# Kernel tuning notes

Measured on AMD Instinct MI355X. Metric: run time of the kernel, lower is better.

## Reference

```python
import jax, jax.numpy as jnp
import numpy as np


def fwht(x):
    """Unnormalized Fast Walsh-Hadamard transform along axis 0 (Sylvester order).
    Equivalent to H @ x where H is the +/-1 Hadamard matrix. x.shape[0] must be a power of 2."""
    D = x.shape[0]
    orig_shape = x.shape
    x = x.reshape(D, -1)
    h = 1
    while h < D:
        x = x.reshape(D // (2 * h), 2, h, -1)
        a = x[:, 0]
        b = x[:, 1]
        x = jnp.stack([a + b, a - b], axis=1)
        h *= 2
    return x.reshape(orig_shape)


def setup_inputs() -> dict:
    D = 4096
    B = 2048
    key = jax.random.key(0)
    k_x, k_eps, k_rho = jax.random.split(key, 3)
    x = jax.random.normal(k_x, (B, D), dtype=jnp.float32)
    epsilon = jax.random.normal(k_eps, (D,), dtype=jnp.float32)
    s1 = jnp.ones((D,), dtype=jnp.float32) * 0.01
    s2 = jnp.ones((D,), dtype=jnp.float32) * 0.01
    g_mu = jnp.zeros((D,), dtype=jnp.float32)
    # g_rho ~ Uniform(-5, -4) as in the torch init
    g_rho = jax.random.uniform(k_rho, (D,), dtype=jnp.float32, minval=-5.0, maxval=-4.0)
    return {"x": x, "epsilon": epsilon, "s1": s1, "s2": s2, "g_mu": g_mu, "g_rho": g_rho}


def reference(x, epsilon, s1, s2, g_mu, g_rho):
    D = s1.shape[0]
    # g_sigma_sqrt_diagonal = softplus(g_rho); sampled diag g = g_mu + sigma * eps.
    # W = diag(s1) @ H @ diag(g) @ H @ diag(s2); mu and sigma terms are linear in g, so combine.
    g = g_mu + jax.nn.softplus(g_rho) * epsilon
    # HS2 = H * s2 (columns of H scaled by s2) = H @ diag(s2) = fwht(diag(s2)) along axis 0
    HS2 = fwht(jnp.diag(s2))                      # [D, D]
    W = s1[:, None] * fwht(g[:, None] * HS2)      # [D, D]
    # F.linear(x, W) = x @ W^T
    return x @ W.T
```

## Files before the change

### kernel.cpp

```cpp
#include <hip/hip_runtime.h>
#include <math.h>

#define DIM 4096
#define ROWS 2048
#define LSTR 65

__device__ __forceinline__ float4 f4mul(float4 a, float4 b) {
    return make_float4(a.x * b.x, a.y * b.y, a.z * b.z, a.w * b.w);
}

__device__ __forceinline__ void fwht_ri(float4 v[16]) {
#pragma unroll
    for (int j = 0; j < 16; ++j) {
        float4 a = v[j];
        float t0 = a.x + a.y, t1 = a.x - a.y;
        float t2 = a.z + a.w, t3 = a.z - a.w;
        v[j] = make_float4(t0 + t2, t1 + t3, t0 - t2, t1 - t3);
    }
#pragma unroll
    for (int m = 1; m < 16; m <<= 1) {
#pragma unroll
        for (int j = 0; j < 16; ++j) {
            if (!(j & m)) {
                int k = j | m;
                float4 a = v[j], b = v[k];
                v[j] = make_float4(a.x + b.x, a.y + b.y, a.z + b.z, a.w + b.w);
                v[k] = make_float4(a.x - b.x, a.y - b.y, a.z - b.z, a.w - b.w);
            }
        }
    }
}

__device__ __forceinline__ void fwht_m(float f[64]) {
#pragma unroll
    for (int s = 0; s < 6; ++s) {
        const int h = 1 << s;
#pragma unroll
        for (int m = 0; m < 64; ++m) {
            if (!(m & h)) {
                const int k = m | h;
                float a = f[m], b = f[k];
                f[m] = a + b;
                f[k] = a - b;
            }
        }
    }
}

__global__ void __launch_bounds__(256, 2)
whvi_main(const float* __restrict__ x, const float* __restrict__ s1,
          const float* __restrict__ s2, const float* __restrict__ eps,
          const float* __restrict__ g_mu, const float* __restrict__ g_rho,
          float* __restrict__ out) {
    const int lane = threadIdx.x & 63;
    const int wid  = threadIdx.x >> 6;
    const int row  = blockIdx.x * 4 + wid;

    __shared__ float lds[4 * 64 * LSTR];
    float* __restrict__ L = lds + wid * 64 * LSTR;

    const float4* __restrict__ xr  = (const float4*)(x + (size_t)row * DIM);
    float4* __restrict__       orw = (float4*)(out + (size_t)row * DIM);
    const float4* __restrict__ s2v = (const float4*)s2;
    const float4* __restrict__ s1v = (const float4*)s1;

    float f[64];
    float4* F = (float4*)f;

#pragma unroll
    for (int r = 0; r < 16; ++r)
        F[r] = f4mul(xr[64 * r + lane], s2v[64 * r + lane]);

    fwht_ri(F);

#pragma unroll
    for (int c = 0; c < 64; ++c)
        L[lane * LSTR + c] = f[c];
#pragma unroll
    for (int m = 0; m < 64; ++m)
        f[m] = L[m * LSTR + lane];

    fwht_m(f);

    {
        const int base = 256 * (lane >> 2) + (lane & 3);
#pragma unroll
        for (int m = 0; m < 64; ++m) {
            const int j = base + 4 * m;
            float u  = __expf(g_rho[j]);
            float sp = __logf(1.0f + u);
            f[m] *= fmaf(sp, eps[j], g_mu[j]);
        }
    }

    fwht_m(f);

#pragma unroll
    for (int m = 0; m < 64; ++m)
        L[lane * LSTR + m] = f[m];
#pragma unroll
    for (int c = 0; c < 64; ++c)
        f[c] = L[c * LSTR + lane];

    fwht_ri(F);

#pragma unroll
    for (int r = 0; r < 16; ++r)
        orw[64 * r + lane] = f4mul(F[r], s1v[64 * r + lane]);
}

extern "C" void kernel_launch(void* const* d_in, const int* in_sizes, int n_in,
                              void* d_out, int out_size, void* d_ws, size_t ws_size,
                              hipStream_t stream) {
    const float* x     = (const float*)d_in[0];
    const float* eps   = (const float*)d_in[1];
    const float* s1    = (const float*)d_in[2];
    const float* s2    = (const float*)d_in[3];
    const float* g_mu  = (const float*)d_in[4];
    const float* g_rho = (const float*)d_in[5];
    float* out = (float*)d_out;

    whvi_main<<<ROWS / 4, 256, 0, stream>>>(x, s1, s2, eps, g_mu, g_rho, out);
}
```

Measured before the change: 106.1 us.

## Precompute diagonal g in a pre-pass kernel and vectorize LDS transposes

A small kernel now computes the diagonal g = g_mu + softplus(g_rho)*eps once, stored in workspace in a lane-contiguous permuted layout. The main kernel reads it as float4 instead of redoing exp/log and three strided scalar loads per element in every row. The LDS row stride changes from 65 to 68 so the row-wise stores can use 128-bit writes, and the occupancy hint in launch_bounds is dropped. The cost is an extra kernel launch, a workspace dependency, and possible bank conflicts on the column reads with the new stride.

```diff
diff --git a/kernel.cpp b/kernel.cpp
--- a/kernel.cpp
+++ b/kernel.cpp
@@ -3,7 +3,18 @@
 
 #define DIM 4096
 #define ROWS 2048
-#define LSTR 65
+#define LSTR 68
+
+__global__ void g_precompute(const float* __restrict__ eps,
+                             const float* __restrict__ g_mu,
+                             const float* __restrict__ g_rho,
+                             float* __restrict__ g_t) {
+    int t = blockIdx.x * blockDim.x + threadIdx.x;
+    int l = t >> 6, m = t & 63;
+    int j = 256 * (l >> 2) + 4 * m + (l & 3);
+    float sp = log1pf(expf(g_rho[j]));
+    g_t[t] = g_mu[j] + sp * eps[j];
+}
 
 __device__ __forceinline__ float4 f4mul(float4 a, float4 b) {
     return make_float4(a.x * b.x, a.y * b.y, a.z * b.z, a.w * b.w);
@@ -47,10 +58,9 @@
     }
 }
 
-__global__ void __launch_bounds__(256, 2)
+__global__ void __launch_bounds__(256)
 whvi_main(const float* __restrict__ x, const float* __restrict__ s1,
-          const float* __restrict__ s2, const float* __restrict__ eps,
-          const float* __restrict__ g_mu, const float* __restrict__ g_rho,
+          const float* __restrict__ s2, const float* __restrict__ g_t,
           float* __restrict__ out) {
     const int lane = threadIdx.x & 63;
     const int wid  = threadIdx.x >> 6;
@@ -58,11 +68,13 @@
 
     __shared__ float lds[4 * 64 * LSTR];
     float* __restrict__ L = lds + wid * 64 * LSTR;
+    float4* __restrict__ L4 = (float4*)(L);
 
     const float4* __restrict__ xr  = (const float4*)(x + (size_t)row * DIM);
     float4* __restrict__       orw = (float4*)(out + (size_t)row * DIM);
     const float4* __restrict__ s2v = (const float4*)s2;
     const float4* __restrict__ s1v = (const float4*)s1;
+    const float4* __restrict__ gtv = (const float4*)g_t;
 
     float f[64];
     float4* F = (float4*)f;
@@ -74,30 +86,23 @@
     fwht_ri(F);
 
 #pragma unroll
-    for (int c = 0; c < 64; ++c)
-        L[lane * LSTR + c] = f[c];
+    for (int r = 0; r < 16; ++r)
+        L4[lane * (LSTR / 4) + r] = F[r];
 #pragma unroll
     for (int m = 0; m < 64; ++m)
         f[m] = L[m * LSTR + lane];
 
     fwht_m(f);
 
-    {
-        const int base = 256 * (lane >> 2) + (lane & 3);
 #pragma unroll
-        for (int m = 0; m < 64; ++m) {
-            const int j = base + 4 * m;
-            float u  = __expf(g_rho[j]);
-            float sp = __logf(1.0f + u);
-            f[m] *= fmaf(sp, eps[j], g_mu[j]);
-        }
-    }
+    for (int k = 0; k < 16; ++k)
+        F[k] = f4mul(F[k], gtv[lane * 16 + k]);
 
     fwht_m(f);
 
 #pragma unroll
-    for (int m = 0; m < 64; ++m)
-        L[lane * LSTR + m] = f[m];
+    for (int k = 0; k < 16; ++k)
+        L4[lane * (LSTR / 4) + k] = F[k];
 #pragma unroll
     for (int c = 0; c < 64; ++c)
         f[c] = L[c * LSTR + lane];
@@ -119,6 +124,8 @@
     const float* g_mu  = (const float*)d_in[4];
     const float* g_rho = (const float*)d_in[5];
     float* out = (float*)d_out;
+    float* g_t = (float*)d_ws;
 
-    whvi_main<<<ROWS / 4, 256, 0, stream>>>(x, s1, s2, eps, g_mu, g_rho, out);
+    g_precompute<<<DIM / 256, 256, 0, stream>>>(eps, g_mu, g_rho, g_t);
+    whvi_main<<<ROWS / 4, 256, 0, stream>>>(x, s1, s2, g_t, out);
 }
```

Result: no change. 104.3 us (-1.7%).

## Precompute diagonal g into shared memory, vectorize LDS writes, shrink blocks

Applied to the files above, without the earlier changes.

Each block now computes the sampled diagonal g (softplus of g_rho times eps plus g_mu) once into a padded shared-memory table. The per-element strided global loads and transcendentals in the scaling step become LDS reads. The transpose stride is padded to 68 so register rows can be written as float4. Blocks drop to two waves of 128 threads with no min-blocks hint, and the g table is recomputed per block, which adds redundant exp/log work and a barrier.

```diff
diff --git a/kernel.cpp b/kernel.cpp
--- a/kernel.cpp
+++ b/kernel.cpp
@@ -3,7 +3,10 @@
 
 #define DIM 4096
 #define ROWS 2048
-#define LSTR 65
+#define LSTR 68
+
+#define GPAD(e) ((e) + ((e) >> 6))
+#define GSZ (DIM + DIM / 64)
 
 __device__ __forceinline__ float4 f4mul(float4 a, float4 b) {
     return make_float4(a.x * b.x, a.y * b.y, a.z * b.z, a.w * b.w);
@@ -47,17 +50,19 @@
     }
 }
 
-__global__ void __launch_bounds__(256, 2)
+__global__ void __launch_bounds__(128)
 whvi_main(const float* __restrict__ x, const float* __restrict__ s1,
           const float* __restrict__ s2, const float* __restrict__ eps,
           const float* __restrict__ g_mu, const float* __restrict__ g_rho,
           float* __restrict__ out) {
     const int lane = threadIdx.x & 63;
     const int wid  = threadIdx.x >> 6;
-    const int row  = blockIdx.x * 4 + wid;
+    const int row  = blockIdx.x * 2 + wid;
 
-    __shared__ float lds[4 * 64 * LSTR];
-    float* __restrict__ L = lds + wid * 64 * LSTR;
+    __shared__ float lds[2 * 64 * LSTR];
+    __shared__ float Lg[GSZ];
+    float* __restrict__ L  = lds + wid * 64 * LSTR;
+    float4* __restrict__ L4 = (float4*)L;
 
     const float4* __restrict__ xr  = (const float4*)(x + (size_t)row * DIM);
     float4* __restrict__       orw = (float4*)(out + (size_t)row * DIM);
@@ -71,11 +76,29 @@
     for (int r = 0; r < 16; ++r)
         F[r] = f4mul(xr[64 * r + lane], s2v[64 * r + lane]);
 
+    {
+        const float4* __restrict__ e4 = (const float4*)eps;
+        const float4* __restrict__ m4 = (const float4*)g_mu;
+        const float4* __restrict__ r4 = (const float4*)g_rho;
+#pragma unroll
+        for (int k = 0; k < 8; ++k) {
+            const int fi = threadIdx.x + 128 * k;
+            const int e0 = 4 * fi;
+            float4 ev = e4[fi], mv = m4[fi], rv = r4[fi];
+            const int w0 = GPAD(e0);
+            Lg[w0 + 0] = fmaf(log1pf(expf(rv.x)), ev.x, mv.x);
+            Lg[w0 + 1] = fmaf(log1pf(expf(rv.y)), ev.y, mv.y);
+            Lg[w0 + 2] = fmaf(log1pf(expf(rv.z)), ev.z, mv.z);
+            Lg[w0 + 3] = fmaf(log1pf(expf(rv.w)), ev.w, mv.w);
+        }
+    }
+    __syncthreads();
+
     fwht_ri(F);
 
 #pragma unroll
-    for (int c = 0; c < 64; ++c)
-        L[lane * LSTR + c] = f[c];
+    for (int r = 0; r < 16; ++r)
+        L4[lane * (LSTR / 4) + r] = F[r];
 #pragma unroll
     for (int m = 0; m < 64; ++m)
         f[m] = L[m * LSTR + lane];
@@ -86,18 +109,16 @@
         const int base = 256 * (lane >> 2) + (lane & 3);
 #pragma unroll
         for (int m = 0; m < 64; ++m) {
-            const int j = base + 4 * m;
-            float u  = __expf(g_rho[j]);
-            float sp = __logf(1.0f + u);
-            f[m] *= fmaf(sp, eps[j], g_mu[j]);
+            const int e = base + 4 * m;
+            f[m] *= Lg[GPAD(e)];
         }
     }
 
     fwht_m(f);
 
 #pragma unroll
-    for (int m = 0; m < 64; ++m)
-        L[lane * LSTR + m] = f[m];
+    for (int k = 0; k < 16; ++k)
+        L4[lane * (LSTR / 4) + k] = F[k];
 #pragma unroll
     for (int c = 0; c < 64; ++c)
         f[c] = L[c * LSTR + lane];
@@ -120,5 +141,5 @@
     const float* g_rho = (const float*)d_in[5];
     float* out = (float*)d_out;
 
-    whvi_main<<<ROWS / 4, 256, 0, stream>>>(x, s1, s2, eps, g_mu, g_rho, out);
+    whvi_main<<<ROWS / 2, 128, 0, stream>>>(x, s1, s2, eps, g_mu, g_rho, out);
 }
```

Result: slower. 115.3 us (+8.7%).
